# Optimization experiments

Measured on AMD Instinct MI355X. Metric: run time of the kernel, lower is better.

The kernel has to match this reference:

```python
import jax, jax.numpy as jnp
import numpy as np

N = 100000
IN_DIM = 128
HID = 256
OUT_DIM = 128
E = 600000


def setup_inputs() -> dict:
    key = jax.random.key(0)
    ks = jax.random.split(key, 10)
    x = jax.random.normal(ks[0], (N, IN_DIM), dtype=jnp.float32)
    edge_index = jax.random.randint(ks[1], (2, E), 0, N, dtype=jnp.int32)

    def lin(k, fan_in, fan_out):
        kw, kb = jax.random.split(k)
        bound = 1.0 / np.sqrt(fan_in)
        W = jax.random.uniform(kw, (fan_in, fan_out), minval=-bound, maxval=bound, dtype=jnp.float32)
        b = jax.random.uniform(kb, (fan_out,), minval=-bound, maxval=bound, dtype=jnp.float32)
        return W, b

    W1a, b1a = lin(ks[2], IN_DIM, HID)
    W1b, b1b = lin(ks[3], HID, HID)
    W2a, b2a = lin(ks[4], HID, HID)
    W2b, b2b = lin(ks[5], HID, OUT_DIM)
    return {"x": x, "edge_index": edge_index,
            "W1a": W1a, "b1a": b1a, "W1b": W1b, "b1b": b1b,
            "W2a": W2a, "b2a": b2a, "W2b": W2b, "b2b": b2b}


def _gin_conv(x, src, dst, Wa, ba, Wb, bb):
    # GINConv with eps=0: h = (1+eps)*x + sum_{j in N(i)} x_j, then 2-layer MLP
    agg = jax.ops.segment_sum(x[src], dst, num_segments=N)  # [N, F]
    h = x + agg
    h = jax.nn.relu(h @ Wa + ba)
    return h @ Wb + bb


def reference(x, edge_index, W1a, b1a, W1b, b1b, W2a, b2a, W2b, b2b):
    src, dst = edge_index[0], edge_index[1]
    h = jax.nn.relu(_gin_conv(x, src, dst, W1a, b1a, W1b, b1b))
    h = jax.nn.relu(_gin_conv(h, src, dst, W2a, b2a, W2b, b2b))
    return h
```

## Files before the change

kernel.cpp:

```cpp
#include <hip/hip_runtime.h>
#include <stdint.h>

#define N_NODES 100000
#define E_EDGES 600000
#define IN_F    128
#define HID_F   256
#define OUT_F   128
#define NB_SCAN 98

typedef unsigned short ushort_t;
typedef short  short8  __attribute__((ext_vector_type(8)));
typedef float  floatx4 __attribute__((ext_vector_type(4)));

__device__ __forceinline__ float bf2f(unsigned u16) {
    return __uint_as_float(u16 << 16);
}
__device__ __forceinline__ ushort_t f2bf(float f) {
    unsigned u = __float_as_uint(f);
    return (ushort_t)((u + 0x7fffu + ((u >> 16) & 1u)) >> 16);
}

__global__ void k_prep(const float* __restrict__ x, ushort_t* __restrict__ xbf,
                       const float* __restrict__ W1a, const float* __restrict__ W1b,
                       const float* __restrict__ W2a, const float* __restrict__ W2b,
                       ushort_t* __restrict__ WT1a, ushort_t* __restrict__ WT1b,
                       ushort_t* __restrict__ WT2a, ushort_t* __restrict__ WT2b,
                       int* __restrict__ cursor, ushort_t* __restrict__ P) {
    int t = blockIdx.x * 256 + threadIdx.x;
    if (t < N_NODES * IN_F / 2) {
        float2 v = ((const float2*)x)[t];
        ((unsigned*)xbf)[t] = (unsigned)f2bf(v.x) | ((unsigned)f2bf(v.y) << 16);
    }
    if (t < N_NODES) cursor[t] = 0;
    if (t < 128) ((unsigned*)(P + (size_t)N_NODES * HID_F))[t] = 0;
    if (t < 64)  ((unsigned*)(xbf + (size_t)N_NODES * IN_F))[t] = 0;
    if (t < 32768) {
        int k = t >> 8, n = t & 255;
        WT1a[n * 128 + k] = f2bf(W1a[t]);
    } else if (t < 98304) {
        int i = t - 32768, k = i >> 8, n = i & 255;
        WT1b[n * 256 + k] = f2bf(W1b[i]);
    } else if (t < 163840) {
        int i = t - 98304, k = i >> 8, n = i & 255;
        WT2a[n * 256 + k] = f2bf(W2a[i]);
    } else if (t < 196608) {
        int i = t - 163840, k = i >> 7, n = i & 127;
        WT2b[n * 256 + k] = f2bf(W2b[i]);
    }
}

__global__ void k_hist(const int* __restrict__ dst, int* __restrict__ deg) {
    int e = blockIdx.x * 256 + threadIdx.x;
    if (e < E_EDGES) atomicAdd(&deg[dst[e]], 1);
}

__global__ void k_scan1(const int* __restrict__ deg, int* __restrict__ row_ptr,
                        int* __restrict__ psum) {
    __shared__ int s[1024];
    int t = threadIdx.x, i = blockIdx.x * 1024 + t;
    int v = (i < N_NODES) ? deg[i] : 0;
    s[t] = v;
    __syncthreads();
    for (int off = 1; off < 1024; off <<= 1) {
        int u = (t >= off) ? s[t - off] : 0;
        __syncthreads();
        if (t >= off) s[t] += u;
        __syncthreads();
    }
    if (i < N_NODES) row_ptr[i] = s[t] - v;
    if (t == 1023) psum[blockIdx.x] = s[t];
}

__global__ void k_scan3(int* __restrict__ row_ptr, const int* __restrict__ psum,
                        int* __restrict__ cursor) {
    __shared__ int pr[128];
    int t = threadIdx.x;
    if (t < 128) pr[t] = (t < blockIdx.x && t < NB_SCAN) ? psum[t] : 0;
    __syncthreads();
    for (int off = 64; off > 0; off >>= 1) {
        if (t < off) pr[t] += pr[t + off];
        __syncthreads();
    }
    const int pre = pr[0];
    int i = blockIdx.x * 1024 + t;
    if (i < N_NODES) {
        int r = row_ptr[i] + pre;
        row_ptr[i] = r;
        cursor[i]  = r;
    }
    if (i == 0) row_ptr[N_NODES] = E_EDGES;
}

__global__ void k_fill(const int* __restrict__ src, const int* __restrict__ dst,
                       int* __restrict__ cursor, int* __restrict__ colidx) {
    int e = blockIdx.x * 256 + threadIdx.x;
    if (e < E_EDGES) {
        int pos = atomicAdd(&cursor[dst[e]], 1);
        colidx[pos] = src[e];
    }
}

__global__ void k_agg128(const ushort_t* __restrict__ Xbf, const int* __restrict__ row_ptr,
                         const int* __restrict__ colidx, ushort_t* __restrict__ Out) {
    int node = blockIdx.x * 4 + (threadIdx.x >> 6);
    int lane = threadIdx.x & 63;
    int q = lane >> 4, l4 = lane & 15;
    const uint4* xr = (const uint4*)Xbf;
    uint4 u = xr[(size_t)node * 16 + l4];
    float a0 = q ? 0.f : bf2f(u.x & 0xffffu);
    float a1 = q ? 0.f : bf2f(u.x >> 16);
    float a2 = q ? 0.f : bf2f(u.y & 0xffffu);
    float a3 = q ? 0.f : bf2f(u.y >> 16);
    float a4 = q ? 0.f : bf2f(u.z & 0xffffu);
    float a5 = q ? 0.f : bf2f(u.z >> 16);
    float a6 = q ? 0.f : bf2f(u.w & 0xffffu);
    float a7 = q ? 0.f : bf2f(u.w >> 16);
    int r0 = row_ptr[node], r1 = row_ptr[node + 1];
    for (int base = r0 + q; base < r1; base += 8) {
        int j0 = colidx[base];
        int j1 = colidx[min(base + 4, r1 - 1)];
        j1 = (base + 4 < r1) ? j1 : N_NODES;
        uint4 w0 = xr[(size_t)j0 * 16 + l4];
        uint4 w1 = xr[(size_t)j1 * 16 + l4];
        a0 += bf2f(w0.x & 0xffffu) + bf2f(w1.x & 0xffffu);
        a1 += bf2f(w0.x >> 16)     + bf2f(w1.x >> 16);
        a2 += bf2f(w0.y & 0xffffu) + bf2f(w1.y & 0xffffu);
        a3 += bf2f(w0.y >> 16)     + bf2f(w1.y >> 16);
        a4 += bf2f(w0.z & 0xffffu) + bf2f(w1.z & 0xffffu);
        a5 += bf2f(w0.z >> 16)     + bf2f(w1.z >> 16);
        a6 += bf2f(w0.w & 0xffffu) + bf2f(w1.w & 0xffffu);
        a7 += bf2f(w0.w >> 16)     + bf2f(w1.w >> 16);
    }
    a0 += __shfl_xor(a0, 16, 64); a0 += __shfl_xor(a0, 32, 64);
    a1 += __shfl_xor(a1, 16, 64); a1 += __shfl_xor(a1, 32, 64);
    a2 += __shfl_xor(a2, 16, 64); a2 += __shfl_xor(a2, 32, 64);
    a3 += __shfl_xor(a3, 16, 64); a3 += __shfl_xor(a3, 32, 64);
    a4 += __shfl_xor(a4, 16, 64); a4 += __shfl_xor(a4, 32, 64);
    a5 += __shfl_xor(a5, 16, 64); a5 += __shfl_xor(a5, 32, 64);
    a6 += __shfl_xor(a6, 16, 64); a6 += __shfl_xor(a6, 32, 64);
    a7 += __shfl_xor(a7, 16, 64); a7 += __shfl_xor(a7, 32, 64);
    if (q == 0) {
        uint4 o;
        o.x = (unsigned)f2bf(a0) | ((unsigned)f2bf(a1) << 16);
        o.y = (unsigned)f2bf(a2) | ((unsigned)f2bf(a3) << 16);
        o.z = (unsigned)f2bf(a4) | ((unsigned)f2bf(a5) << 16);
        o.w = (unsigned)f2bf(a6) | ((unsigned)f2bf(a7) << 16);
        ((uint4*)Out)[(size_t)node * 16 + l4] = o;
    }
}

__global__ void k_agg256(const ushort_t* __restrict__ X, const int* __restrict__ row_ptr,
                         const int* __restrict__ colidx, ushort_t* __restrict__ Out) {
    int node = blockIdx.x * 4 + (threadIdx.x >> 6);
    int lane = threadIdx.x & 63;
    int h = lane >> 5, l5 = lane & 31;
    const uint4* xr = (const uint4*)X;
    uint4 u = xr[(size_t)node * 32 + l5];
    float a0 = h ? 0.f : bf2f(u.x & 0xffffu);
    float a1 = h ? 0.f : bf2f(u.x >> 16);
    float a2 = h ? 0.f : bf2f(u.y & 0xffffu);
    float a3 = h ? 0.f : bf2f(u.y >> 16);
    float a4 = h ? 0.f : bf2f(u.z & 0xffffu);
    float a5 = h ? 0.f : bf2f(u.z >> 16);
    float a6 = h ? 0.f : bf2f(u.w & 0xffffu);
    float a7 = h ? 0.f : bf2f(u.w >> 16);
    int r0 = row_ptr[node], r1 = row_ptr[node + 1];
    for (int base = r0 + h; base < r1; base += 8) {
        int j0 = colidx[base];
        int j1 = colidx[min(base + 2, r1 - 1)];
        int j2 = colidx[min(base + 4, r1 - 1)];
        int j3 = colidx[min(base + 6, r1 - 1)];
        j1 = (base + 2 < r1) ? j1 : N_NODES;
        j2 = (base + 4 < r1) ? j2 : N_NODES;
        j3 = (base + 6 < r1) ? j3 : N_NODES;
        uint4 w0 = xr[(size_t)j0 * 32 + l5];
        uint4 w1 = xr[(size_t)j1 * 32 + l5];
        uint4 w2 = xr[(size_t)j2 * 32 + l5];
        uint4 w3 = xr[(size_t)j3 * 32 + l5];
        a0 += (bf2f(w0.x & 0xffffu) + bf2f(w1.x & 0xffffu)) +
              (bf2f(w2.x & 0xffffu) + bf2f(w3.x & 0xffffu));
        a1 += (bf2f(w0.x >> 16) + bf2f(w1.x >> 16)) +
              (bf2f(w2.x >> 16) + bf2f(w3.x >> 16));
        a2 += (bf2f(w0.y & 0xffffu) + bf2f(w1.y & 0xffffu)) +
              (bf2f(w2.y & 0xffffu) + bf2f(w3.y & 0xffffu));
        a3 += (bf2f(w0.y >> 16) + bf2f(w1.y >> 16)) +
              (bf2f(w2.y >> 16) + bf2f(w3.y >> 16));
        a4 += (bf2f(w0.z & 0xffffu) + bf2f(w1.z & 0xffffu)) +
              (bf2f(w2.z & 0xffffu) + bf2f(w3.z & 0xffffu));
        a5 += (bf2f(w0.z >> 16) + bf2f(w1.z >> 16)) +
              (bf2f(w2.z >> 16) + bf2f(w3.z >> 16));
        a6 += (bf2f(w0.w & 0xffffu) + bf2f(w1.w & 0xffffu)) +
              (bf2f(w2.w & 0xffffu) + bf2f(w3.w & 0xffffu));
        a7 += (bf2f(w0.w >> 16) + bf2f(w1.w >> 16)) +
              (bf2f(w2.w >> 16) + bf2f(w3.w >> 16));
    }
    a0 += __shfl_xor(a0, 32, 64);
    a1 += __shfl_xor(a1, 32, 64);
    a2 += __shfl_xor(a2, 32, 64);
    a3 += __shfl_xor(a3, 32, 64);
    a4 += __shfl_xor(a4, 32, 64);
    a5 += __shfl_xor(a5, 32, 64);
    a6 += __shfl_xor(a6, 32, 64);
    a7 += __shfl_xor(a7, 32, 64);
    if (h == 0) {
        uint4 o;
        o.x = (unsigned)f2bf(a0) | ((unsigned)f2bf(a1) << 16);
        o.y = (unsigned)f2bf(a2) | ((unsigned)f2bf(a3) << 16);
        o.z = (unsigned)f2bf(a4) | ((unsigned)f2bf(a5) << 16);
        o.w = (unsigned)f2bf(a6) | ((unsigned)f2bf(a7) << 16);
        ((uint4*)Out)[(size_t)node * 32 + l5] = o;
    }
}

template <int FIN, int FOUT, bool OUT_F32>
__global__ __launch_bounds__(512, 4) void gemm_relu(
    const ushort_t* __restrict__ Act, const ushort_t* __restrict__ WT,
    const float* __restrict__ bias, void* __restrict__ Out, int nRows)
{
    constexpr int CPR = FIN / 8;
    constexpr int KC  = FIN / 32;
    constexpr int KP  = KC / 2;
    constexpr int SW  = 136;
    constexpr int WTE = 128 * FIN;
    constexpr int EPE = 128 * SW;
    __shared__ ushort_t wt[(WTE > EPE) ? WTE : EPE];

    const int tid  = threadIdx.x;
    const int bid  = blockIdx.x;

    int rowblk, sl;
    if (FOUT == 256) {
        const int group = bid >> 4, w = bid & 15;
        rowblk = group * 8 + (w & 7);
        sl     = w >> 3;
        if (rowblk >= (nRows + 255) / 256) return;
    } else {
        rowblk = bid;
        sl     = 0;
    }
    const int slab = sl * 128;

    {
        const ushort_t* wsrc = WT + (size_t)slab * FIN;
#pragma unroll
        for (int rr = 0; rr < (128 * CPR) / 512; ++rr) {
            int ci  = rr * 512 + tid;
            int n   = ci / CPR;
            int csw = ci % CPR;
            int cor = csw ^ (n & 15);
            const ushort_t* g = wsrc + (size_t)n * FIN + cor * 8;
            __builtin_amdgcn_global_load_lds(
                (const __attribute__((address_space(1))) unsigned*)g,
                (__attribute__((address_space(3))) unsigned*)&wt[ci * 8],
                16, 0, 0);
        }
    }

    const int wave = tid >> 6, lane = tid & 63;
    const int quad = lane >> 4, l15 = lane & 15;
    const int rowBase = rowblk * 256 + wave * 32;

    int r0 = rowBase + l15;
    int r1 = r0 + 16;
    r0 = (r0 < nRows) ? r0 : (nRows - 1);
    r1 = (r1 < nRows) ? r1 : (nRows - 1);
    const ushort_t* a0p = Act + (size_t)r0 * FIN + quad * 8;
    const ushort_t* a1p = Act + (size_t)r1 * FIN + quad * 8;

    short8 af[2][2][2];
#pragma unroll
    for (int kc = 0; kc < 2; ++kc) {
        af[0][0][kc] = *(const short8*)(a0p + kc * 32);
        af[0][1][kc] = *(const short8*)(a1p + kc * 32);
    }

    floatx4 acc[2][8];
#pragma unroll
    for (int mt = 0; mt < 2; ++mt)
#pragma unroll
        for (int nt = 0; nt < 8; ++nt)
#pragma unroll
            for (int r = 0; r < 4; ++r) acc[mt][nt][r] = 0.f;

    __syncthreads();

#pragma unroll
    for (int p = 0; p < KP; ++p) {
        const int cb = p & 1, nb = cb ^ 1;
        if (p + 1 < KP) {
#pragma unroll
            for (int kc = 0; kc < 2; ++kc) {
                af[nb][0][kc] = *(const short8*)(a0p + ((p + 1) * 2 + kc) * 32);
                af[nb][1][kc] = *(const short8*)(a1p + ((p + 1) * 2 + kc) * 32);
            }
        }
#pragma unroll
        for (int kc = 0; kc < 2; ++kc) {
            int chunk = (p * 2 + kc) * 4 + quad;
#pragma unroll
            for (int nt = 0; nt < 8; ++nt) {
                int n = nt * 16 + l15;
                int csw = chunk ^ (n & 15);
                short8 bfr = *(const short8*)&wt[n * FIN + csw * 8];
                acc[0][nt] = __builtin_amdgcn_mfma_f32_16x16x32_bf16(af[cb][0][kc], bfr, acc[0][nt], 0, 0, 0);
                acc[1][nt] = __builtin_amdgcn_mfma_f32_16x16x32_bf16(af[cb][1][kc], bfr, acc[1][nt], 0, 0, 0);
            }
        }
    }

    if (!OUT_F32) {
        const int rowTileBase = rowblk * 256;
#pragma unroll
        for (int mt = 0; mt < 2; ++mt) {
            __syncthreads();
#pragma unroll
            for (int nt = 0; nt < 8; ++nt) {
                int col = slab + nt * 16 + l15;
                float bv = bias[col];
#pragma unroll
                for (int r = 0; r < 4; ++r) {
                    float v = fmaxf(acc[mt][nt][r] + bv, 0.f);
                    wt[(wave * 16 + quad * 4 + r) * SW + nt * 16 + l15] = f2bf(v);
                }
            }
            __syncthreads();
#pragma unroll
            for (int it = 0; it < 4; ++it) {
                int idx = it * 512 + tid;
                int gr  = idx >> 4;
                int c   = idx & 15;
                int row = rowTileBase + (gr >> 4) * 32 + mt * 16 + (gr & 15);
                uint4 vv = *(const uint4*)&wt[gr * SW + c * 8];
                if (row < nRows)
                    *(uint4*)((ushort_t*)Out + (size_t)row * FOUT + slab + c * 8) = vv;
            }
        }
    } else {
#pragma unroll
        for (int mt = 0; mt < 2; ++mt) {
#pragma unroll
            for (int nt = 0; nt < 8; ++nt) {
                int col = slab + nt * 16 + l15;
                float bv = bias[col];
#pragma unroll
                for (int r = 0; r < 4; ++r) {
                    int row = rowBase + mt * 16 + quad * 4 + r;
                    if (row < nRows) {
                        float v = fmaxf(acc[mt][nt][r] + bv, 0.f);
                        ((float*)Out)[(size_t)row * FOUT + col] = v;
                    }
                }
            }
        }
    }
}

extern "C" void kernel_launch(void* const* d_in, const int* in_sizes, int n_in,
                              void* d_out, int out_size, void* d_ws, size_t ws_size,
                              hipStream_t stream) {
    const float* x   = (const float*)d_in[0];
    const int*   ei  = (const int*)d_in[1];
    const int*   src = ei;
    const int*   dst = ei + E_EDGES;
    const float* W1a = (const float*)d_in[2];
    const float* b1a = (const float*)d_in[3];
    const float* W1b = (const float*)d_in[4];
    const float* b1b = (const float*)d_in[5];
    const float* W2a = (const float*)d_in[6];
    const float* b2a = (const float*)d_in[7];
    const float* W2b = (const float*)d_in[8];
    const float* b2b = (const float*)d_in[9];

    const size_t NP1 = N_NODES + 1;
    ushort_t* P       = (ushort_t*)d_ws;
    ushort_t* Q       = P + NP1 * HID_F;
    ushort_t* xbf     = Q;
    int*      row_ptr = (int*)(Q + NP1 * HID_F);
    int*      cursor  = row_ptr + (N_NODES + 4);
    int*      colidx  = cursor + N_NODES;
    int*      psum    = colidx + E_EDGES;
    ushort_t* WT1a    = (ushort_t*)(psum + 128);
    ushort_t* WT1b    = WT1a + 256 * 128;
    ushort_t* WT2a    = WT1b + 256 * 256;
    ushort_t* WT2b    = WT2a + 256 * 256;

    k_prep<<<(N_NODES * IN_F / 2 + 255) / 256, 256, 0, stream>>>(
        x, xbf, W1a, W1b, W2a, W2b, WT1a, WT1b, WT2a, WT2b, cursor, P);

    k_hist <<<(E_EDGES + 255) / 256, 256, 0, stream>>>(dst, cursor);
    k_scan1<<<NB_SCAN, 1024, 0, stream>>>(cursor, row_ptr, psum);
    k_scan3<<<NB_SCAN, 1024, 0, stream>>>(row_ptr, psum, cursor);
    k_fill <<<(E_EDGES + 255) / 256, 256, 0, stream>>>(src, dst, cursor, colidx);

    const int ROWB = (N_NODES + 255) / 256;
    const int GP   = ((ROWB + 7) / 8) * 16;

    k_agg128<<<N_NODES / 4, 256, 0, stream>>>(xbf, row_ptr, colidx, P);
    gemm_relu<128, 256, false><<<GP, 512, 0, stream>>>(P, WT1a, b1a, Q, N_NODES);
    gemm_relu<256, 256, false><<<GP, 512, 0, stream>>>(Q, WT1b, b1b, P, N_NODES);

    k_agg256<<<N_NODES / 4, 256, 0, stream>>>(P, row_ptr, colidx, Q);
    gemm_relu<256, 256, false><<<GP, 512, 0, stream>>>(Q, WT2a, b2a, P, N_NODES);
    gemm_relu<256, 128, true><<<ROWB, 512, 0, stream>>>(P, WT2b, b2b, d_out, N_NODES);
}
```

Before: 367.5 us.

## Stage GEMM weight slab in two 64-column halves to halve LDS footprint

The GEMM kernel now loads the 128-column weight slab into LDS as two 64-column halves, running the full K loop over each half in turn and accumulating into the matching accumulator columns. This halves the weight LDS allocation (and the f32-output variant no longer reserves epilogue space), which is meant to let more blocks reside per CU. In exchange the activation rows are re-read from global memory twice and an extra barrier plus weight reload is added between halves.

```diff
diff --git a/kernel.cpp b/kernel.cpp
--- a/kernel.cpp
+++ b/kernel.cpp
@@ -221,9 +221,10 @@
     constexpr int KC  = FIN / 32;
     constexpr int KP  = KC / 2;
     constexpr int SW  = 136;
-    constexpr int WTE = 128 * FIN;
+    constexpr int WHE = 64 * FIN;
     constexpr int EPE = 128 * SW;
-    __shared__ ushort_t wt[(WTE > EPE) ? WTE : EPE];
+    constexpr int LDSE = OUT_F32 ? WHE : ((WHE > EPE) ? WHE : EPE);
+    __shared__ ushort_t wt[LDSE];
 
     const int tid  = threadIdx.x;
     const int bid  = blockIdx.x;
@@ -240,22 +241,6 @@
     }
     const int slab = sl * 128;
 
-    {
-        const ushort_t* wsrc = WT + (size_t)slab * FIN;
-#pragma unroll
-        for (int rr = 0; rr < (128 * CPR) / 512; ++rr) {
-            int ci  = rr * 512 + tid;
-            int n   = ci / CPR;
-            int csw = ci % CPR;
-            int cor = csw ^ (n & 15);
-            const ushort_t* g = wsrc + (size_t)n * FIN + cor * 8;
-            __builtin_amdgcn_global_load_lds(
-                (const __attribute__((address_space(1))) unsigned*)g,
-                (__attribute__((address_space(3))) unsigned*)&wt[ci * 8],
-                16, 0, 0);
-        }
-    }
-
     const int wave = tid >> 6, lane = tid & 63;
     const int quad = lane >> 4, l15 = lane & 15;
     const int rowBase = rowblk * 256 + wave * 32;
@@ -267,13 +252,6 @@
     const ushort_t* a0p = Act + (size_t)r0 * FIN + quad * 8;
     const ushort_t* a1p = Act + (size_t)r1 * FIN + quad * 8;
 
-    short8 af[2][2][2];
-#pragma unroll
-    for (int kc = 0; kc < 2; ++kc) {
-        af[0][0][kc] = *(const short8*)(a0p + kc * 32);
-        af[0][1][kc] = *(const short8*)(a1p + kc * 32);
-    }
-
     floatx4 acc[2][8];
 #pragma unroll
     for (int mt = 0; mt < 2; ++mt)
@@ -282,28 +260,56 @@
 #pragma unroll
             for (int r = 0; r < 4; ++r) acc[mt][nt][r] = 0.f;
 
-    __syncthreads();
-
-#pragma unroll
-    for (int p = 0; p < KP; ++p) {
-        const int cb = p & 1, nb = cb ^ 1;
-        if (p + 1 < KP) {
+#pragma unroll
+    for (int hs = 0; hs < 2; ++hs) {
+        if (hs) __syncthreads();
+
+        {
+            const ushort_t* wsrc = WT + (size_t)(slab + hs * 64) * FIN;
+#pragma unroll
+            for (int rr = 0; rr < (64 * CPR) / 512; ++rr) {
+                int ci  = rr * 512 + tid;
+                int nl  = ci / CPR;
+                int csw = ci % CPR;
+                int cor = csw ^ (nl & 15);
+                const ushort_t* g = wsrc + (size_t)nl * FIN + cor * 8;
+                __builtin_amdgcn_global_load_lds(
+                    (const __attribute__((address_space(1))) unsigned*)g,
+                    (__attribute__((address_space(3))) unsigned*)&wt[ci * 8],
+                    16, 0, 0);
+            }
+        }
+
+        short8 af[2][2][2];
+#pragma unroll
+        for (int kc = 0; kc < 2; ++kc) {
+            af[0][0][kc] = *(const short8*)(a0p + kc * 32);
+            af[0][1][kc] = *(const short8*)(a1p + kc * 32);
+        }
+
+        __syncthreads();
+
+#pragma unroll
+        for (int p = 0; p < KP; ++p) {
+            const int cb = p & 1, nb = cb ^ 1;
+            if (p + 1 < KP) {
+#pragma unroll
+                for (int kc = 0; kc < 2; ++kc) {
+                    af[nb][0][kc] = *(const short8*)(a0p + ((p + 1) * 2 + kc) * 32);
+                    af[nb][1][kc] = *(const short8*)(a1p + ((p + 1) * 2 + kc) * 32);
+                }
+            }
 #pragma unroll
             for (int kc = 0; kc < 2; ++kc) {
-                af[nb][0][kc] = *(const short8*)(a0p + ((p + 1) * 2 + kc) * 32);
-                af[nb][1][kc] = *(const short8*)(a1p + ((p + 1) * 2 + kc) * 32);
-            }
-        }
-#pragma unroll
-        for (int kc = 0; kc < 2; ++kc) {
-            int chunk = (p * 2 + kc) * 4 + quad;
-#pragma unroll
-            for (int nt = 0; nt < 8; ++nt) {
-                int n = nt * 16 + l15;
-                int csw = chunk ^ (n & 15);
-                short8 bfr = *(const short8*)&wt[n * FIN + csw * 8];
-                acc[0][nt] = __builtin_amdgcn_mfma_f32_16x16x32_bf16(af[cb][0][kc], bfr, acc[0][nt], 0, 0, 0);
-                acc[1][nt] = __builtin_amdgcn_mfma_f32_16x16x32_bf16(af[cb][1][kc], bfr, acc[1][nt], 0, 0, 0);
+                int chunk = (p * 2 + kc) * 4 + quad;
+#pragma unroll
+                for (int nt = 0; nt < 4; ++nt) {
+                    int nl  = nt * 16 + l15;
+                    int csw = chunk ^ (nl & 15);
+                    short8 bfr = *(const short8*)&wt[nl * FIN + csw * 8];
+                    acc[0][hs * 4 + nt] = __builtin_amdgcn_mfma_f32_16x16x32_bf16(af[cb][0][kc], bfr, acc[0][hs * 4 + nt], 0, 0, 0);
+                    acc[1][hs * 4 + nt] = __builtin_amdgcn_mfma_f32_16x16x32_bf16(af[cb][1][kc], bfr, acc[1][hs * 4 + nt], 0, 0, 0);
+                }
             }
         }
     }
@@ -314,13 +320,14 @@
         for (int mt = 0; mt < 2; ++mt) {
             __syncthreads();
 #pragma unroll
-            for (int nt = 0; nt < 8; ++nt) {
-                int col = slab + nt * 16 + l15;
+            for (int j = 0; j < 8; ++j) {
+                int colLocal = (j >> 2) * 64 + (j & 3) * 16 + l15;
+                int col = slab + colLocal;
                 float bv = bias[col];
 #pragma unroll
                 for (int r = 0; r < 4; ++r) {
-                    float v = fmaxf(acc[mt][nt][r] + bv, 0.f);
-                    wt[(wave * 16 + quad * 4 + r) * SW + nt * 16 + l15] = f2bf(v);
+                    float v = fmaxf(acc[mt][j][r] + bv, 0.f);
+                    wt[(wave * 16 + quad * 4 + r) * SW + colLocal] = f2bf(v);
                 }
             }
             __syncthreads();
@@ -339,14 +346,14 @@
 #pragma unroll
         for (int mt = 0; mt < 2; ++mt) {
 #pragma unroll
-            for (int nt = 0; nt < 8; ++nt) {
-                int col = slab + nt * 16 + l15;
+            for (int j = 0; j < 8; ++j) {
+                int col = slab + (j >> 2) * 64 + (j & 3) * 16 + l15;
                 float bv = bias[col];
 #pragma unroll
                 for (int r = 0; r < 4; ++r) {
                     int row = rowBase + mt * 16 + quad * 4 + r;
                     if (row < nRows) {
-                        float v = fmaxf(acc[mt][nt][r] + bv, 0.f);
+                        float v = fmaxf(acc[mt][j][r] + bv, 0.f);
                         ((float*)Out)[(size_t)row * FOUT + col] = v;
                     }
                 }
```

Result: slower. 398.2 us (+8.4%).
